# Kernel optimization log

Measured on AMD Instinct MI355X. Metric: run time of the kernel, lower is better.

The kernel has to match this reference:

```python
import jax, jax.numpy as jnp
import numpy as np

HEADS = 16
DIM_HEAD = 64
QUERY_DIM = 1024
INNER_DIM = HEADS * DIM_HEAD  # 1024
SCALE = DIM_HEAD ** -0.5


def setup_inputs() -> dict:
    key = jax.random.key(0)
    ks = jax.random.split(key, 6)
    B, S = 2, 2048
    hidden_states = jax.random.normal(ks[0], (B, S, QUERY_DIM), dtype=jnp.float32)
    # torch Linear weights are [out, in]; store transposed [in, out] for x @ W
    w_q = jax.random.normal(ks[1], (QUERY_DIM, INNER_DIM), dtype=jnp.float32) * (QUERY_DIM ** -0.5)
    w_k = jax.random.normal(ks[2], (QUERY_DIM, INNER_DIM), dtype=jnp.float32) * (QUERY_DIM ** -0.5)
    w_v = jax.random.normal(ks[3], (QUERY_DIM, INNER_DIM), dtype=jnp.float32) * (QUERY_DIM ** -0.5)
    w_o = jax.random.normal(ks[4], (INNER_DIM, QUERY_DIM), dtype=jnp.float32) * (INNER_DIM ** -0.5)
    b_o = jax.random.normal(ks[5], (QUERY_DIM,), dtype=jnp.float32) * 0.01
    return {"hidden_states": hidden_states, "w_q": w_q, "w_k": w_k, "w_v": w_v, "w_o": w_o, "b_o": b_o}


def reference(hidden_states, w_q, w_k, w_v, w_o, b_o):
    B, S, _ = hidden_states.shape
    # QKV projections (context = hidden_states, i.e. self-attention)
    q = (hidden_states @ w_q).reshape(B, S, HEADS, DIM_HEAD)
    k = (hidden_states @ w_k).reshape(B, S, HEADS, DIM_HEAD)
    v = (hidden_states @ w_v).reshape(B, S, HEADS, DIM_HEAD)
    # scaled dot-product attention; scores materialized as [B, H, S, S]
    scores = jnp.einsum("bqhd,bkhd->bhqk", q, k) * SCALE
    probs = jax.nn.softmax(scores, axis=-1)
    out = jnp.einsum("bhqk,bkhd->bqhd", probs, v).reshape(B, S, INNER_DIM)
    return out @ w_o + b_o
```

## Files before the change

kernel.cpp:

```cpp
#include <hip/hip_runtime.h>
#include <cstdint>
#include <cstddef>

typedef unsigned short u16;
typedef unsigned int u32;
typedef __bf16 bf16x8 __attribute__((ext_vector_type(8)));
typedef float f32x4 __attribute__((ext_vector_type(4)));
typedef float f32x16 __attribute__((ext_vector_type(16)));
typedef u32 u32x2 __attribute__((ext_vector_type(2)));
typedef u32 u32x4 __attribute__((ext_vector_type(4)));

#define AS1 __attribute__((address_space(1)))
#define AS3 __attribute__((address_space(3)))

__device__ __forceinline__ void gld16(const u16* g, u16* l) {
  __builtin_amdgcn_global_load_lds((const AS1 void*)(const void*)g,
                                   (AS3 void*)(void*)l, 16, 0, 0);
}

__device__ __forceinline__ u16 f2bf(float f) {
  union { float f; unsigned u; } x; x.f = f;
  return (u16)((x.u + 0x7fffu + ((x.u >> 16) & 1u)) >> 16);
}

__device__ __forceinline__ float fexp2(float x) {
  float r; asm("v_exp_f32 %0, %1" : "=v"(r) : "v"(x)); return r;
}

__device__ __forceinline__ f32x16 zf16() {
  f32x16 v;
#pragma unroll
  for (int i = 0; i < 16; ++i) v[i] = 0.f;
  return v;
}

__device__ __forceinline__ bf16x8 mk8(u32x2 a, u32x2 b) {
  union { u32x4 u; bf16x8 v; } x;
  x.u[0] = a[0]; x.u[1] = a[1]; x.u[2] = b[0]; x.u[3] = b[1];
  return x.v;
}

__global__ void k_prep(const float* __restrict__ X,
                       const float* __restrict__ wq, const float* __restrict__ wk,
                       const float* __restrict__ wv, const float* __restrict__ wo,
                       u16* __restrict__ Xb, u16* __restrict__ Wqkv, u16* __restrict__ Wot) {
  const int z = blockIdx.z;
  if (z == 4) {
    int bid = blockIdx.y * 32 + blockIdx.x;
    int tid = threadIdx.y * 32 + threadIdx.x;
#pragma unroll
    for (int k = 0; k < 4; ++k) {
      int i = bid * 1024 + k * 256 + tid;
      float4 v = reinterpret_cast<const float4*>(X)[i];
      ushort4 o;
      o.x = f2bf(v.x); o.y = f2bf(v.y); o.z = f2bf(v.z); o.w = f2bf(v.w);
      reinterpret_cast<ushort4*>(Xb)[i] = o;
    }
    return;
  }
  __shared__ float t[32][33];
  const float* in = (z == 0) ? wq : (z == 1) ? wk : (z == 2) ? wv : wo;
  u16* out = (z < 3) ? (Wqkv + (size_t)z * 1048576) : Wot;
  int bx = blockIdx.x * 32, by = blockIdx.y * 32;
  int tx = threadIdx.x, ty = threadIdx.y;
#pragma unroll
  for (int j = 0; j < 32; j += 8)
    t[ty + j][tx] = in[(size_t)(by + ty + j) * 1024 + bx + tx];
  __syncthreads();
#pragma unroll
  for (int j = 0; j < 32; j += 8)
    out[(size_t)(bx + ty + j) * 1024 + by + tx] = f2bf(t[tx][ty + j]);
}

__global__ __launch_bounds__(256) void k_gemm_qkv(
    const u16* __restrict__ Xb,
    const u16* __restrict__ Wt,
    u16* __restrict__ Qb,
    u16* __restrict__ Kb,
    u16* __restrict__ Vt) {
  __shared__ __align__(16) u16 As[128][32];
  __shared__ __align__(16) u16 Bs[128][32];
  const int tid = threadIdx.x;
  const int w = tid >> 6, l = tid & 63;
  const int bm = blockIdx.x * 128;
  const int bn = blockIdx.y * 128;
  const int wm = (w >> 1) * 64, wn = (w & 1) * 64;
  const int lm = l & 15, lg = l >> 4;

  f32x4 acc[4][4];
#pragma unroll
  for (int i = 0; i < 4; ++i)
#pragma unroll
    for (int j = 0; j < 4; ++j) acc[i][j] = f32x4{0.f, 0.f, 0.f, 0.f};

  const int srow = w * 16 + (l >> 2);
  const int scol = (l & 3) * 8;
  for (int k0 = 0; k0 < 1024; k0 += 32) {
#pragma unroll
    for (int j = 0; j < 2; ++j) {
      gld16(Xb + (size_t)(bm + j * 64 + srow) * 1024 + k0 + scol, &As[j * 64 + w * 16][0]);
      gld16(Wt + (size_t)(bn + j * 64 + srow) * 1024 + k0 + scol, &Bs[j * 64 + w * 16][0]);
    }
    __syncthreads();
    bf16x8 af[4], bfr[4];
#pragma unroll
    for (int mt = 0; mt < 4; ++mt)
      af[mt] = *reinterpret_cast<const bf16x8*>(&As[wm + mt * 16 + lm][lg * 8]);
#pragma unroll
    for (int nt = 0; nt < 4; ++nt)
      bfr[nt] = *reinterpret_cast<const bf16x8*>(&Bs[wn + nt * 16 + lm][lg * 8]);
#pragma unroll
    for (int mt = 0; mt < 4; ++mt)
#pragma unroll
      for (int nt = 0; nt < 4; ++nt)
        acc[mt][nt] = __builtin_amdgcn_mfma_f32_16x16x32_bf16(af[mt], bfr[nt], acc[mt][nt], 0, 0, 0);
    __syncthreads();
  }
#pragma unroll
  for (int nt = 0; nt < 4; ++nt) {
    int gc = bn + wn + nt * 16 + lm;
    int which = gc >> 10, jc = gc & 1023, h = jc >> 6, d = jc & 63;
#pragma unroll
    for (int mt = 0; mt < 4; ++mt) {
#pragma unroll
      for (int r = 0; r < 4; ++r) {
        int gr = bm + wm + mt * 16 + lg * 4 + r;
        int b = gr >> 11, s = gr & 2047;
        float v = acc[mt][nt][r];
        size_t bh = (size_t)(b * 16 + h);
        if (which == 0)      Qb[(bh * 2048 + s) * 64 + d] = f2bf(v * 0.18033688f);
        else if (which == 1) Kb[(bh * 2048 + s) * 64 + d] = f2bf(v);
        else                 Vt[(bh * 64 + d) * 2048 + s] = f2bf(v);
      }
    }
  }
}

__global__ __launch_bounds__(256) void k_attn(
    const u16* __restrict__ Qb, const u16* __restrict__ Kb,
    const u16* __restrict__ Vt, u16* __restrict__ Ab) {
  __shared__ __align__(16) u16 Ks[2][4224];
  __shared__ __align__(16) u16 Vs[2][4224];
  __shared__ float lb[4][32];
  const int tid = threadIdx.x, w = tid >> 6, l = tid & 63;
  const int lm = l & 31, hi = l >> 5;
  const int kx = lm & 7;
  const int bh = blockIdx.x;
  const int q0 = blockIdx.y * 128 + w * 32;
  const u16* Qh = Qb + (size_t)bh * 2048 * 64;
  const u16* Kh = Kb + (size_t)bh * 2048 * 64;
  const u16* Vh = Vt + (size_t)bh * 64 * 2048;

  bf16x8 qf[4];
#pragma unroll
  for (int c = 0; c < 4; ++c)
    qf[c] = *reinterpret_cast<const bf16x8*>(&Qh[(size_t)(q0 + lm) * 64 + 16 * c + 8 * hi]);

  f32x16 o0 = zf16(), o1 = zf16();
  float lsum = 0.f;

  const int sr8 = l >> 3;
  const int sg = l & 7;
  const int koff = (lm >> 3) * 528 + (lm & 7) * 64;

#define STAGE(tile, buf)                                                          \
  {                                                                               \
    const int kvn_ = (tile) * 64;                                                 \
    _Pragma("unroll")                                                             \
    for (int j = 0; j < 2; ++j) {                                                 \
      int row_ = w * 16 + j * 8 + sr8;                                            \
      int g_ = sg ^ sr8;                                                          \
      gld16(Kh + (size_t)(kvn_ + row_) * 64 + 8 * g_, &Ks[buf][(w * 2 + j) * 528]); \
      gld16(Vh + (size_t)row_ * 2048 + kvn_ + 8 * g_, &Vs[buf][(w * 2 + j) * 528]); \
    }                                                                             \
  }

  STAGE(0, 0);
  __syncthreads();

  for (int t = 0; t < 32; ++t) {
    const int cur = t & 1, nxt = cur ^ 1;

    if (t < 31) STAGE(t + 1, nxt);

    const u16* Kc = &Ks[cur][0];
    bf16x8 pf[2][2];
    float ps0 = 0.f, ps1 = 0.f, ps2 = 0.f, ps3 = 0.f;

    {
      f32x16 st = zf16();
      __builtin_amdgcn_s_setprio(1);
#pragma unroll
      for (int c = 0; c < 4; ++c) {
        bf16x8 kf = *reinterpret_cast<const bf16x8*>(Kc + koff + 8 * ((2 * c + hi) ^ kx));
        st = __builtin_amdgcn_mfma_f32_32x32x16_bf16(kf, qf[c], st, 0, 0, 0);
      }
      __builtin_amdgcn_s_setprio(0);
#pragma unroll
      for (int j = 0; j < 2; ++j)
#pragma unroll
        for (int ii = 0; ii < 8; ++ii) {
          float p = fexp2(st[8 * j + ii]);
          pf[0][j][ii] = (__bf16)p;
          if ((ii & 3) == 0)      ps0 += p;
          else if ((ii & 3) == 1) ps1 += p;
          else if ((ii & 3) == 2) ps2 += p;
          else                    ps3 += p;
        }
    }
    {
      f32x16 st = zf16();
      __builtin_amdgcn_s_setprio(1);
#pragma unroll
      for (int c = 0; c < 4; ++c) {
        bf16x8 kf = *reinterpret_cast<const bf16x8*>(Kc + koff + 2112 + 8 * ((2 * c + hi) ^ kx));
        st = __builtin_amdgcn_mfma_f32_32x32x16_bf16(kf, qf[c], st, 0, 0, 0);
      }
      __builtin_amdgcn_s_setprio(0);
#pragma unroll
      for (int j = 0; j < 2; ++j)
#pragma unroll
        for (int ii = 0; ii < 8; ++ii) {
          float p = fexp2(st[8 * j + ii]);
          pf[1][j][ii] = (__bf16)p;
          if ((ii & 3) == 0)      ps0 += p;
          else if ((ii & 3) == 1) ps1 += p;
          else if ((ii & 3) == 2) ps2 += p;
          else                    ps3 += p;
        }
    }
    float ps = (ps0 + ps1) + (ps2 + ps3);
    ps += __shfl_xor(ps, 32);
    lsum += ps;

    const u16* Vc = &Vs[cur][0];
    __builtin_amdgcn_s_setprio(1);
#pragma unroll
    for (int tt = 0; tt < 2; ++tt)
#pragma unroll
      for (int j = 0; j < 2; ++j) {
        int Ga = 4 * tt + 2 * j;
        u32x2 a0 = *reinterpret_cast<const u32x2*>(Vc + koff + 8 * (Ga ^ kx) + 4 * hi);
        u32x2 a1 = *reinterpret_cast<const u32x2*>(Vc + koff + 8 * ((Ga + 1) ^ kx) + 4 * hi);
        u32x2 b0 = *reinterpret_cast<const u32x2*>(Vc + koff + 2112 + 8 * (Ga ^ kx) + 4 * hi);
        u32x2 b1 = *reinterpret_cast<const u32x2*>(Vc + koff + 2112 + 8 * ((Ga + 1) ^ kx) + 4 * hi);
        o0 = __builtin_amdgcn_mfma_f32_32x32x16_bf16(pf[tt][j], mk8(a0, a1), o0, 0, 0, 0);
        o1 = __builtin_amdgcn_mfma_f32_32x32x16_bf16(pf[tt][j], mk8(b0, b1), o1, 0, 0, 0);
      }
    __builtin_amdgcn_s_setprio(0);

    __syncthreads();
  }
#undef STAGE

  lb[w][lm] = lsum;
  asm volatile("s_waitcnt lgkmcnt(0)" ::: "memory");
  __builtin_amdgcn_sched_barrier(0);
  const int b = bh >> 4, h = bh & 15;
#pragma unroll
  for (int r = 0; r < 16; ++r) {
    int cr = (r & 3) + 8 * (r >> 2) + 4 * hi;
    float inv = 1.0f / lb[w][cr];
    size_t ro = ((size_t)(b * 2048 + q0 + cr)) * 1024 + h * 64;
    Ab[ro + lm]      = f2bf(o0[r] * inv);
    Ab[ro + 32 + lm] = f2bf(o1[r] * inv);
  }
}

__global__ __launch_bounds__(256) void k_gemm_out(
    const u16* __restrict__ Ab,
    const u16* __restrict__ Wot,
    const float* __restrict__ bias, float* __restrict__ out) {
  __shared__ __align__(16) u16 As[128][32];
  __shared__ __align__(16) u16 Bs[128][32];
  const int tid = threadIdx.x;
  const int w = tid >> 6, l = tid & 63;
  const int bm = blockIdx.x * 128;
  const int bn = blockIdx.y * 128;
  const int wm = (w >> 1) * 64, wn = (w & 1) * 64;
  const int lm = l & 15, lg = l >> 4;

  f32x4 acc[4][4];
#pragma unroll
  for (int i = 0; i < 4; ++i)
#pragma unroll
    for (int j = 0; j < 4; ++j) acc[i][j] = f32x4{0.f, 0.f, 0.f, 0.f};

  const int srow = w * 16 + (l >> 2);
  const int scol = (l & 3) * 8;
  for (int k0 = 0; k0 < 1024; k0 += 32) {
#pragma unroll
    for (int j = 0; j < 2; ++j) {
      gld16(Ab  + (size_t)(bm + j * 64 + srow) * 1024 + k0 + scol, &As[j * 64 + w * 16][0]);
      gld16(Wot + (size_t)(bn + j * 64 + srow) * 1024 + k0 + scol, &Bs[j * 64 + w * 16][0]);
    }
    __syncthreads();
    bf16x8 af[4], bfr[4];
#pragma unroll
    for (int mt = 0; mt < 4; ++mt)
      af[mt] = *reinterpret_cast<const bf16x8*>(&As[wm + mt * 16 + lm][lg * 8]);
#pragma unroll
    for (int nt = 0; nt < 4; ++nt)
      bfr[nt] = *reinterpret_cast<const bf16x8*>(&Bs[wn + nt * 16 + lm][lg * 8]);
#pragma unroll
    for (int mt = 0; mt < 4; ++mt)
#pragma unroll
      for (int nt = 0; nt < 4; ++nt)
        acc[mt][nt] = __builtin_amdgcn_mfma_f32_16x16x32_bf16(af[mt], bfr[nt], acc[mt][nt], 0, 0, 0);
    __syncthreads();
  }
#pragma unroll
  for (int nt = 0; nt < 4; ++nt) {
    int gc = bn + wn + nt * 16 + lm;
    float bv = bias[gc];
#pragma unroll
    for (int mt = 0; mt < 4; ++mt) {
#pragma unroll
      for (int r = 0; r < 4; ++r) {
        int gr = bm + wm + mt * 16 + lg * 4 + r;
        out[(size_t)gr * 1024 + gc] = acc[mt][nt][r] + bv;
      }
    }
  }
}

extern "C" void kernel_launch(void* const* d_in, const int* in_sizes, int n_in,
                              void* d_out, int out_size, void* d_ws, size_t ws_size,
                              hipStream_t stream) {
  const float* X  = (const float*)d_in[0];
  const float* wq = (const float*)d_in[1];
  const float* wk = (const float*)d_in[2];
  const float* wv = (const float*)d_in[3];
  const float* wo = (const float*)d_in[4];
  const float* bo = (const float*)d_in[5];
  float* out = (float*)d_out;

  char* ws = (char*)d_ws;
  u16* Xb   = (u16*)(ws);
  u16* Wqkv = (u16*)(ws + (size_t)(8u  << 20));
  u16* Wot  = (u16*)(ws + (size_t)(14u << 20));
  u16* Qb   = (u16*)(ws + (size_t)(16u << 20));
  u16* Kb   = (u16*)(ws + (size_t)(24u << 20));
  u16* Vt   = (u16*)(ws + (size_t)(32u << 20));
  u16* Ab   = (u16*)(ws + (size_t)(40u << 20));

  k_prep<<<dim3(32, 32, 5), dim3(32, 8), 0, stream>>>(X, wq, wk, wv, wo, Xb, Wqkv, Wot);
  k_gemm_qkv<<<dim3(32, 24), 256, 0, stream>>>(Xb, Wqkv, Qb, Kb, Vt);
  k_attn<<<dim3(32, 16), 256, 0, stream>>>(Qb, Kb, Vt, Ab);
  k_gemm_out<<<dim3(32, 8), 256, 0, stream>>>(Ab, Wot, bo, out);
}
```

Baseline: 121.2 us.

## Split attention KV range across two blocks and merge partial outputs

The attention grid gains a z dimension of 2, so each block handles half of the key/value sequence. Blocks now write unnormalized bf16 partial outputs and per-row exp sums to workspace instead of normalized outputs. A new merge kernel adds the two partials, divides by the combined sum, and writes the attention output in the layout the output projection expects. This doubles the block count to raise per-CU occupancy, at the cost of an extra launch, extra global traffic for the partials, and bf16 rounding of unnormalized partial sums.

New measurement: 128.7 us. +6.2%, slower.

```diff
diff --git a/kernel.cpp b/kernel.cpp
--- a/kernel.cpp
+++ b/kernel.cpp
@@ -21,6 +21,10 @@
 __device__ __forceinline__ u16 f2bf(float f) {
   union { float f; unsigned u; } x; x.f = f;
   return (u16)((x.u + 0x7fffu + ((x.u >> 16) & 1u)) >> 16);
+}
+
+__device__ __forceinline__ float bf2f(u16 u) {
+  union { u32 i; float f; } x; x.i = ((u32)u) << 16; return x.f;
 }
 
 __device__ __forceinline__ float fexp2(float x) {
@@ -138,18 +142,20 @@
 
 __global__ __launch_bounds__(256) void k_attn(
     const u16* __restrict__ Qb, const u16* __restrict__ Kb,
-    const u16* __restrict__ Vt, u16* __restrict__ Ab) {
+    const u16* __restrict__ Vt,
+    u16* __restrict__ Opb,
+    float* __restrict__ lsums) {
   __shared__ __align__(16) u16 Ks[2][4224];
   __shared__ __align__(16) u16 Vs[2][4224];
-  __shared__ float lb[4][32];
   const int tid = threadIdx.x, w = tid >> 6, l = tid & 63;
   const int lm = l & 31, hi = l >> 5;
   const int kx = lm & 7;
   const int bh = blockIdx.x;
   const int q0 = blockIdx.y * 128 + w * 32;
+  const int z = blockIdx.z;
   const u16* Qh = Qb + (size_t)bh * 2048 * 64;
-  const u16* Kh = Kb + (size_t)bh * 2048 * 64;
-  const u16* Vh = Vt + (size_t)bh * 64 * 2048;
+  const u16* Kh = Kb + ((size_t)bh * 2048 + z * 1024) * 64;
+  const u16* Vh = Vt + (size_t)bh * 64 * 2048 + z * 1024;
 
   bf16x8 qf[4];
 #pragma unroll
@@ -178,10 +184,10 @@
   STAGE(0, 0);
   __syncthreads();
 
-  for (int t = 0; t < 32; ++t) {
+  for (int t = 0; t < 16; ++t) {
     const int cur = t & 1, nxt = cur ^ 1;
 
-    if (t < 31) STAGE(t + 1, nxt);
+    if (t < 15) STAGE(t + 1, nxt);
 
     const u16* Kc = &Ks[cur][0];
     bf16x8 pf[2][2];
@@ -253,18 +259,36 @@
   }
 #undef STAGE
 
-  lb[w][lm] = lsum;
-  asm volatile("s_waitcnt lgkmcnt(0)" ::: "memory");
-  __builtin_amdgcn_sched_barrier(0);
-  const int b = bh >> 4, h = bh & 15;
+  const size_t robase = ((size_t)z * 32 + bh) * 2048 + q0;
+  if (!hi) lsums[robase + lm] = lsum;
 #pragma unroll
   for (int r = 0; r < 16; ++r) {
     int cr = (r & 3) + 8 * (r >> 2) + 4 * hi;
-    float inv = 1.0f / lb[w][cr];
-    size_t ro = ((size_t)(b * 2048 + q0 + cr)) * 1024 + h * 64;
-    Ab[ro + lm]      = f2bf(o0[r] * inv);
-    Ab[ro + 32 + lm] = f2bf(o1[r] * inv);
-  }
+    size_t ro = (robase + cr) * 64;
+    Opb[ro + lm]      = f2bf(o0[r]);
+    Opb[ro + 32 + lm] = f2bf(o1[r]);
+  }
+}
+
+__global__ __launch_bounds__(256) void k_merge(
+    const u16* __restrict__ Opb, const float* __restrict__ lsums,
+    u16* __restrict__ Ab) {
+  int idx = blockIdx.x * 256 + threadIdx.x;
+  int d8 = idx & 7, q = (idx >> 3) & 2047, bh = idx >> 14;
+  size_t r0 = (size_t)bh * 2048 + q;
+  size_t r1 = (size_t)(32 + bh) * 2048 + q;
+  float inv = 1.0f / (lsums[r0] + lsums[r1]);
+  u32x4 a0 = *reinterpret_cast<const u32x4*>(&Opb[r0 * 64 + d8 * 8]);
+  u32x4 a1 = *reinterpret_cast<const u32x4*>(&Opb[r1 * 64 + d8 * 8]);
+  u32x4 o;
+#pragma unroll
+  for (int j = 0; j < 4; ++j) {
+    float lo = (bf2f((u16)(a0[j] & 0xffff)) + bf2f((u16)(a1[j] & 0xffff))) * inv;
+    float hb = (bf2f((u16)(a0[j] >> 16))    + bf2f((u16)(a1[j] >> 16)))    * inv;
+    o[j] = (u32)f2bf(lo) | ((u32)f2bf(hb) << 16);
+  }
+  int b = bh >> 4, h = bh & 15;
+  *reinterpret_cast<u32x4*>(&Ab[((size_t)b * 2048 + q) * 1024 + h * 64 + d8 * 8]) = o;
 }
 
 __global__ __launch_bounds__(256) void k_gemm_out(
@@ -336,16 +360,19 @@
   float* out = (float*)d_out;
 
   char* ws = (char*)d_ws;
-  u16* Xb   = (u16*)(ws);
-  u16* Wqkv = (u16*)(ws + (size_t)(8u  << 20));
-  u16* Wot  = (u16*)(ws + (size_t)(14u << 20));
-  u16* Qb   = (u16*)(ws + (size_t)(16u << 20));
-  u16* Kb   = (u16*)(ws + (size_t)(24u << 20));
-  u16* Vt   = (u16*)(ws + (size_t)(32u << 20));
-  u16* Ab   = (u16*)(ws + (size_t)(40u << 20));
+  u16*   Xb    = (u16*)(ws);
+  u16*   Wqkv  = (u16*)(ws + (size_t)(8u  << 20));
+  u16*   Wot   = (u16*)(ws + (size_t)(14u << 20));
+  u16*   Qb    = (u16*)(ws + (size_t)(16u << 20));
+  u16*   Kb    = (u16*)(ws + (size_t)(24u << 20));
+  u16*   Vt    = (u16*)(ws + (size_t)(32u << 20));
+  u16*   Opb   = (u16*)(ws + (size_t)(40u << 20));
+  float* lsums = (float*)(ws + (size_t)(8u << 20));
+  u16*   Ab    = (u16*)(ws);
 
   k_prep<<<dim3(32, 32, 5), dim3(32, 8), 0, stream>>>(X, wq, wk, wv, wo, Xb, Wqkv, Wot);
   k_gemm_qkv<<<dim3(32, 24), 256, 0, stream>>>(Xb, Wqkv, Qb, Kb, Vt);
-  k_attn<<<dim3(32, 16), 256, 0, stream>>>(Qb, Kb, Vt, Ab);
+  k_attn<<<dim3(32, 16, 2), 256, 0, stream>>>(Qb, Kb, Vt, Opb, lsums);
+  k_merge<<<2048, 256, 0, stream>>>(Opb, lsums, Ab);
   k_gemm_out<<<dim3(32, 8), 256, 0, stream>>>(Ab, Wot, bo, out);
 }
```
